# Kernel optimization log

Hardware: AMD Instinct MI355X
Metric: run time of the kernel (lower is better)

Reference implementation:

```python
import math
import jax, jax.numpy as jnp
import numpy as np

B, L, D = 1, 2048, 3072
H, KV, HD = 32, 32, 96
THETA = 10000.0
MAXP, ORIGP = 131072, 4096
ROPE_SCALE = math.sqrt(1.0 + math.log(MAXP / ORIGP) / math.log(ORIGP))
ATTN_SCALE = HD ** -0.5
OP = H * HD + 2 * KV * HD  # 9216


def setup_inputs() -> dict:
    key = jax.random.key(0)
    k1, k2, k3, k4 = jax.random.split(key, 4)
    return {
        "x": jax.random.normal(k1, (B, L, D), jnp.float32),
        "w_qkv": jax.random.normal(k2, (OP, D), jnp.float32) * (D ** -0.5),
        "w_o": jax.random.normal(k3, (D, H * HD), jnp.float32) * ((H * HD) ** -0.5),
        # Phi-3 su-scaling short factors are ~1.0; sample near 1
        "short_factor": 1.0 + 0.5 * jax.random.uniform(k4, (HD // 2,), jnp.float32),
    }


def _rotate_half(t):
    t1, t2 = jnp.split(t, 2, axis=-1)
    return jnp.concatenate([-t2, t1], axis=-1)


def reference(x, w_qkv, w_o, short_factor):
    # fused QKV projection
    qkv = x @ w_qkv.T  # [B,L,OP]
    q, k, v = jnp.split(qkv, [H * HD, H * HD + KV * HD], axis=-1)
    q = q.reshape(B, L, H, HD).transpose(0, 2, 1, 3)   # [B,H,L,HD]
    k = k.reshape(B, L, KV, HD).transpose(0, 2, 1, 3)  # [B,KV,L,HD]
    v = v.reshape(B, L, KV, HD).transpose(0, 2, 1, 3)

    # SuRoPE (always uses short_factor, matching source)
    pos = jnp.arange(L, dtype=jnp.float32)  # position_ids default arange
    inv_freq = 1.0 / (short_factor * THETA ** (jnp.arange(0, HD, 2, dtype=jnp.float32) / HD))  # [HD/2]
    freqs = pos[:, None] * inv_freq[None, :]            # [L,HD/2]
    emb = jnp.concatenate([freqs, freqs], axis=-1)      # [L,HD]
    cos = (jnp.cos(emb) * ROPE_SCALE)[None, None]       # [1,1,L,HD]
    sin = (jnp.sin(emb) * ROPE_SCALE)[None, None]
    q = q * cos + _rotate_half(q) * sin
    k = k * cos + _rotate_half(k) * sin

    # causal mask, naive attention (matches source)
    mask = jnp.triu(jnp.full((L, L), -jnp.inf, dtype=jnp.float32), 1)
    scores = jnp.einsum('bhqd,bhkd->bhqk', q * ATTN_SCALE, k) + mask
    attn = jax.nn.softmax(scores, axis=-1)
    o = jnp.einsum('bhqk,bhkd->bhqd', attn, v)
    o = o.transpose(0, 2, 1, 3).reshape(B, L, H * HD)
    return o @ w_o.T
```

## Files before the change

### kernel.cpp

```cpp
#include <hip/hip_runtime.h>
#include <math.h>

typedef __attribute__((ext_vector_type(4))) float f32x4;
typedef __attribute__((ext_vector_type(4))) float f4;
typedef __attribute__((ext_vector_type(8))) _Float16 h8;
typedef __attribute__((ext_vector_type(8))) unsigned short us8;

static __device__ __forceinline__ h8 ld8h(const _Float16* p) {
    return __builtin_bit_cast(h8, *(const us8*)p);
}
static __device__ __forceinline__ void glds16(const void* g, void* l) {
    __builtin_amdgcn_global_load_lds((const __attribute__((address_space(1))) unsigned int*)g,
                                     (__attribute__((address_space(3))) unsigned int*)l, 16, 0, 0);
}

__global__ void convert_half(const float* __restrict__ in, _Float16* __restrict__ out, int n8) {
    int i = blockIdx.x * blockDim.x + threadIdx.x;
    if (i >= n8) return;
    f4 v0 = *(const f4*)(in + (size_t)i * 8);
    f4 v1 = *(const f4*)(in + (size_t)i * 8 + 4);
    h8 o;
#pragma unroll
    for (int j = 0; j < 4; j++) {
        o[j] = (_Float16)v0[j];
        o[j + 4] = (_Float16)v1[j];
    }
    *(h8*)(out + (size_t)i * 8) = o;
}

__global__ void rope_table(const float* __restrict__ sf, float* __restrict__ cs,
                           float* __restrict__ sn, float rope_scale) {
    int i = blockIdx.x * blockDim.x + threadIdx.x;
    const int j = i % 48, l = i / 48;
    const float e = (float)(2 * j) / 96.0f;
    const float inv = 1.0f / (sf[j] * powf(10000.0f, e));
    const float ang = (float)l * inv;
    cs[i] = cosf(ang) * rope_scale;
    sn[i] = sinf(ang) * rope_scale;
}

__global__ __launch_bounds__(256, 3) void gemm_qkv(
    const _Float16* __restrict__ A, const _Float16* __restrict__ B,
    const float* __restrict__ cs, const float* __restrict__ sn,
    _Float16* __restrict__ Qh, _Float16* __restrict__ Kh, _Float16* __restrict__ Vh,
    float attn_scale) {
    const int K = 3072;
    __shared__ _Float16 As[2][128][32], Bs[2][192][32];
    const int t = threadIdx.x;
    const int lane = t & 63, w = t >> 6;
    const int bm = blockIdx.y * 128, bn = blockIdx.x * 192;
    const int wm = w >> 1, wn = w & 1;
    const int l15 = lane & 15, l4 = lane >> 4;

    int car[2], cas[2], cbr[3], cbs[3];
#pragma unroll
    for (int i = 0; i < 2; i++) {
        const int c = t + i * 256;
        car[i] = c >> 2;
        cas[i] = (((c & 3) ^ ((car[i] >> 1) & 3)) * 8);
    }
#pragma unroll
    for (int i = 0; i < 3; i++) {
        const int c = t + i * 256;
        cbr[i] = c >> 2;
        cbs[i] = (((c & 3) ^ ((cbr[i] >> 1) & 3)) * 8);
    }

    f32x4 acc[4][6] = {};

#define STG_QKV(k0_, buf)                                                              \
    {                                                                                  \
        _Float16* ab = &As[(buf)][0][0];                                               \
        _Float16* bb = &Bs[(buf)][0][0];                                               \
        _Pragma("unroll") for (int i = 0; i < 2; i++)                                  \
            glds16(A + (size_t)(bm + car[i]) * K + (k0_) + cas[i], ab + (t + i * 256) * 8); \
        _Pragma("unroll") for (int i = 0; i < 3; i++)                                  \
            glds16(B + (size_t)(bn + cbr[i]) * K + (k0_) + cbs[i], bb + (t + i * 256) * 8); \
    }

    STG_QKV(0, 0)

    int cur = 0;
    for (int k0 = 0; k0 < K; k0 += 32) {
        __syncthreads();
        if (k0 + 32 < K) STG_QKV(k0 + 32, cur ^ 1)
        h8 af[4], bf[6];
#pragma unroll
        for (int m = 0; m < 4; m++) {
            const int row = wm * 64 + m * 16 + l15;
            af[m] = ld8h(&As[cur][row][(l4 ^ ((row >> 1) & 3)) * 8]);
        }
#pragma unroll
        for (int n = 0; n < 6; n++) {
            const int row = wn * 96 + n * 16 + l15;
            bf[n] = ld8h(&Bs[cur][row][(l4 ^ ((row >> 1) & 3)) * 8]);
        }
#pragma unroll
        for (int m = 0; m < 4; m++)
#pragma unroll
            for (int n = 0; n < 6; n++)
                acc[m][n] = __builtin_amdgcn_mfma_f32_16x16x32_f16(af[m], bf[n], acc[m][n], 0, 0, 0);
        cur ^= 1;
    }
#undef STG_QKV

    const int opcol0 = bn + wn * 96;
    const int which = opcol0 / 3072;
    const int h = (opcol0 % 3072) / 96;

    if (which == 2) {
#pragma unroll
        for (int m = 0; m < 4; m++)
#pragma unroll
            for (int r = 0; r < 4; r++) {
                const int l = bm + wm * 64 + m * 16 + l4 * 4 + r;
#pragma unroll
                for (int n = 0; n < 6; n++)
                    Vh[((size_t)h * 2048 + l) * 96 + n * 16 + l15] = (_Float16)acc[m][n][r];
            }
    } else {
        _Float16* dst = (which == 0) ? Qh : Kh;
        const float qs = (which == 0) ? attn_scale : 1.0f;
#pragma unroll
        for (int m = 0; m < 4; m++)
#pragma unroll
            for (int r = 0; r < 4; r++) {
                const int l = bm + wm * 64 + m * 16 + l4 * 4 + r;
                const float* csl = cs + l * 48;
                const float* snl = sn + l * 48;
                const size_t rowb = ((size_t)h * 2048 + l) * 96;
#pragma unroll
                for (int n = 0; n < 3; n++) {
                    const int j = n * 16 + l15;
                    const float c = csl[j], s = snl[j];
                    const float lo = acc[m][n][r], hi = acc[m][n + 3][r];
                    dst[rowb + j] = (_Float16)((lo * c - hi * s) * qs);
                    dst[rowb + j + 48] = (_Float16)((hi * c + lo * s) * qs);
                }
            }
    }
}

template <typename OT>
__global__ __launch_bounds__(256, 3) void gemm_t(
    const _Float16* __restrict__ A, const _Float16* __restrict__ B,
    OT* __restrict__ C, int M, int N, int K) {
    __shared__ _Float16 As[2][128][32], Bs[2][128][32];
    const int t = threadIdx.x;
    const int lane = t & 63, w = t >> 6;
    const int bm = blockIdx.y * 128, bn = blockIdx.x * 128;
    const int wy = w >> 1, wx = w & 1;
    const int l15 = lane & 15, l4 = lane >> 4;

    const int c0 = (w * 2 + 0) * 64 + lane;
    const int c1 = (w * 2 + 1) * 64 + lane;
    const int r0s = c0 >> 2, s0 = (((c0 & 3) ^ ((r0s >> 1) & 3)) * 8);
    const int r1s = c1 >> 2, s1 = (((c1 & 3) ^ ((r1s >> 1) & 3)) * 8);

    f32x4 acc[4][4] = {};

    glds16(A + (size_t)(bm + r0s) * K + s0, &As[0][0][0] + c0 * 8);
    glds16(A + (size_t)(bm + r1s) * K + s1, &As[0][0][0] + c1 * 8);
    glds16(B + (size_t)(bn + r0s) * K + s0, &Bs[0][0][0] + c0 * 8);
    glds16(B + (size_t)(bn + r1s) * K + s1, &Bs[0][0][0] + c1 * 8);

    int cry[4], crx[4];
#pragma unroll
    for (int m = 0; m < 4; m++) {
        const int rowA = wy * 64 + m * 16 + l15;
        cry[m] = ((l4 ^ ((rowA >> 1) & 3)) * 8);
        const int rowB = wx * 64 + m * 16 + l15;
        crx[m] = ((l4 ^ ((rowB >> 1) & 3)) * 8);
    }

    int cur = 0;
    for (int k0 = 0; k0 < K; k0 += 32) {
        __syncthreads();
        const int nk = k0 + 32;
        if (nk < K) {
            _Float16* an = &As[cur ^ 1][0][0];
            _Float16* bn_ = &Bs[cur ^ 1][0][0];
            glds16(A + (size_t)(bm + r0s) * K + nk + s0, an + c0 * 8);
            glds16(A + (size_t)(bm + r1s) * K + nk + s1, an + c1 * 8);
            glds16(B + (size_t)(bn + r0s) * K + nk + s0, bn_ + c0 * 8);
            glds16(B + (size_t)(bn + r1s) * K + nk + s1, bn_ + c1 * 8);
        }
        h8 af[4], bf[4];
#pragma unroll
        for (int m = 0; m < 4; m++) af[m] = ld8h(&As[cur][wy * 64 + m * 16 + l15][cry[m]]);
#pragma unroll
        for (int n = 0; n < 4; n++) bf[n] = ld8h(&Bs[cur][wx * 64 + n * 16 + l15][crx[n]]);
#pragma unroll
        for (int m = 0; m < 4; m++)
#pragma unroll
            for (int n = 0; n < 4; n++)
                acc[m][n] = __builtin_amdgcn_mfma_f32_16x16x32_f16(af[m], bf[n], acc[m][n], 0, 0, 0);
        cur ^= 1;
    }

#pragma unroll
    for (int m = 0; m < 4; m++)
#pragma unroll
        for (int n = 0; n < 4; n++)
#pragma unroll
            for (int r = 0; r < 4; r++)
                C[(size_t)(bm + wy * 64 + m * 16 + l4 * 4 + r) * N + bn + wx * 64 + n * 16 + l15] =
                    (OT)acc[m][n][r];
}

__global__ __launch_bounds__(256) void vtrans(const _Float16* __restrict__ Vh,
                                              _Float16* __restrict__ Vt) {
    __shared__ _Float16 tile[64][105];
    const int h = blockIdx.y;
    const int l0 = blockIdx.x * 64;
    const int t = threadIdx.x;
#pragma unroll
    for (int i = 0; i < 3; i++) {
        const int v = t + i * 256;
        const int row = v / 12, seg = (v % 12) * 8;
        *(us8*)&tile[row][seg] =
            *(const us8*)(Vh + ((size_t)h * 2048 + l0 + row) * 96 + seg);
    }
    __syncthreads();
#pragma unroll
    for (int i = 0; i < 3; i++) {
        const int v = t + i * 256;
        const int d = v >> 3, lc = v & 7;
        h8 o;
#pragma unroll
        for (int j = 0; j < 8; j++) o[j] = tile[lc * 8 + j][d];
        *(h8*)(Vt + ((size_t)h * 96 + d) * 2048 + l0 + lc * 8) = o;
    }
}

__global__ __launch_bounds__(512, 2) void attn_mfma(
    const _Float16* __restrict__ Qh, const _Float16* __restrict__ Kh,
    const _Float16* __restrict__ Vt, _Float16* __restrict__ Oh) {
    __shared__ _Float16 Ks[2][64][104];
    __shared__ _Float16 Vs[2][96][72];
    __shared__ _Float16 Ps[8][16][72];

    const int h = blockIdx.y;
    const int qt = 7 - (int)blockIdx.x;
    const int q0 = qt * 256;
    const int t = threadIdx.x, lane = t & 63, w = t >> 6;
    const int l15 = lane & 15, l4 = lane >> 4;
    const int wq = q0 + w * 32;

    const _Float16* Kg = Kh + (size_t)h * 2048 * 96;
    const _Float16* Vg = Vt + (size_t)h * 96 * 2048;

    h8 qf[2][3];
#pragma unroll
    for (int g = 0; g < 2; g++) {
        const size_t qrow = ((size_t)h * 2048 + wq + g * 16 + l15) * 96;
#pragma unroll
        for (int kc = 0; kc < 3; kc++) qf[g][kc] = ld8h(Qh + qrow + kc * 32 + l4 * 8);
    }

    const int cA = t, rKA = cA / 12, sKA = (cA % 12) * 8;
    const int rVA = cA >> 3, sVA = (cA & 7) * 8;
    const int cB = 512 + t, rKB = cB / 12, sKB = (cB % 12) * 8;
    const int rVB = cB >> 3, sVB = (cB & 7) * 8;
    const bool two = (t < 256);

    us8 kregA, vregA, kregB, vregB;
    kregA = *(const us8*)(Kg + (size_t)rKA * 96 + sKA);
    vregA = *(const us8*)(Vg + (size_t)rVA * 2048 + sVA);
    if (two) {
        kregB = *(const us8*)(Kg + (size_t)rKB * 96 + sKB);
        vregB = *(const us8*)(Vg + (size_t)rVB * 2048 + sVB);
    }

    f32x4 o[2][6] = {};
    float m_i[2][4], l_i[2][4];
#pragma unroll
    for (int g = 0; g < 2; g++)
#pragma unroll
        for (int r = 0; r < 4; r++) { m_i[g][r] = -1e30f; l_i[g][r] = 0.f; }

    const int nkt = 4 * qt + 4;
    for (int kt = 0; kt < nkt; kt++) {
        const int kv0 = kt * 64;
        const int buf = kt & 1;
        *(us8*)&Ks[buf][rKA][sKA] = kregA;
        *(us8*)&Vs[buf][rVA][sVA] = vregA;
        if (two) {
            *(us8*)&Ks[buf][rKB][sKB] = kregB;
            *(us8*)&Vs[buf][rVB][sVB] = vregB;
        }
        __syncthreads();
        if (kt + 1 < nkt) {
            const int kv1 = kv0 + 64;
            kregA = *(const us8*)(Kg + (size_t)(kv1 + rKA) * 96 + sKA);
            vregA = *(const us8*)(Vg + (size_t)rVA * 2048 + kv1 + sVA);
            if (two) {
                kregB = *(const us8*)(Kg + (size_t)(kv1 + rKB) * 96 + sKB);
                vregB = *(const us8*)(Vg + (size_t)rVB * 2048 + kv1 + sVB);
            }
        }

        if (kv0 <= wq + 31) {
            f32x4 s[2][4] = {};
#pragma unroll
            for (int f = 0; f < 4; f++)
#pragma unroll
                for (int kc = 0; kc < 3; kc++) {
                    h8 kf = ld8h(&Ks[buf][f * 16 + l15][kc * 32 + l4 * 8]);
#pragma unroll
                    for (int g = 0; g < 2; g++)
                        s[g][f] = __builtin_amdgcn_mfma_f32_16x16x32_f16(qf[g][kc], kf, s[g][f], 0, 0, 0);
                }

            if (kv0 + 63 > wq) {
#pragma unroll
                for (int g = 0; g < 2; g++)
#pragma unroll
                    for (int f = 0; f < 4; f++)
#pragma unroll
                        for (int r = 0; r < 4; r++)
                            if (kv0 + f * 16 + l15 > wq + g * 16 + l4 * 4 + r) s[g][f][r] = -1e30f;
            }

            float mx[2][4];
#pragma unroll
            for (int g = 0; g < 2; g++)
#pragma unroll
                for (int r = 0; r < 4; r++) {
                    float m0 = fmaxf(fmaxf(s[g][0][r], s[g][1][r]), fmaxf(s[g][2][r], s[g][3][r]));
#pragma unroll
                    for (int msk = 1; msk < 16; msk <<= 1) m0 = fmaxf(m0, __shfl_xor(m0, msk, 64));
                    mx[g][r] = m0;
                }

            bool need = false;
#pragma unroll
            for (int g = 0; g < 2; g++)
#pragma unroll
                for (int r = 0; r < 4; r++) need = need || (mx[g][r] > m_i[g][r] + 8.0f);
            if (__any(need)) {
#pragma unroll
                for (int g = 0; g < 2; g++)
#pragma unroll
                    for (int r = 0; r < 4; r++) {
                        const float mnew = fmaxf(m_i[g][r], mx[g][r]);
                        const float sc = __expf(m_i[g][r] - mnew);
                        m_i[g][r] = mnew;
                        l_i[g][r] *= sc;
#pragma unroll
                        for (int f2 = 0; f2 < 6; f2++) o[g][f2][r] *= sc;
                    }
            }

#pragma unroll
            for (int g = 0; g < 2; g++) {
#pragma unroll
                for (int f = 0; f < 4; f++)
#pragma unroll
                    for (int r = 0; r < 4; r++) {
                        const float p = __expf(s[g][f][r] - m_i[g][r]);
                        Ps[w][l4 * 4 + r][f * 16 + l15] = (_Float16)p;
                        l_i[g][r] += p;
                    }
#pragma unroll
                for (int kc2 = 0; kc2 < 2; kc2++) {
                    h8 pa = ld8h(&Ps[w][l15][kc2 * 32 + l4 * 8]);
#pragma unroll
                    for (int f2 = 0; f2 < 6; f2++) {
                        h8 vb = ld8h(&Vs[buf][f2 * 16 + l15][kc2 * 32 + l4 * 8]);
                        o[g][f2] = __builtin_amdgcn_mfma_f32_16x16x32_f16(pa, vb, o[g][f2], 0, 0, 0);
                    }
                }
            }
        }
    }

#pragma unroll
    for (int g = 0; g < 2; g++)
#pragma unroll
        for (int r = 0; r < 4; r++) {
            float ss = l_i[g][r];
#pragma unroll
            for (int msk = 1; msk < 16; msk <<= 1) ss += __shfl_xor(ss, msk, 64);
            const float inv = 1.0f / ss;
            const size_t row = (size_t)(wq + g * 16 + l4 * 4 + r) * 3072 + h * 96;
#pragma unroll
            for (int f2 = 0; f2 < 6; f2++)
                Oh[row + f2 * 16 + l15] = (_Float16)(o[g][f2][r] * inv);
        }
}

extern "C" void kernel_launch(void* const* d_in, const int* in_sizes, int n_in,
                              void* d_out, int out_size, void* d_ws, size_t ws_size,
                              hipStream_t stream) {
    const float* x = (const float*)d_in[0];
    const float* w_qkv = (const float*)d_in[1];
    const float* w_o = (const float*)d_in[2];
    const float* sf = (const float*)d_in[3];
    float* out = (float*)d_out;
    char* ws = (char*)d_ws;

    _Float16* wqkvh = (_Float16*)(ws);
    _Float16* Qh = (_Float16*)(ws + 56623104);
    _Float16* Kh = (_Float16*)(ws + 69206016);
    _Float16* Vh = (_Float16*)(ws + 81788928);
    _Float16* Vth = (_Float16*)(ws + 94371840);
    _Float16* Oh = (_Float16*)(ws + 106954752);
    _Float16* xh = (_Float16*)(ws + 132120576);
    _Float16* woh = (_Float16*)(ws + 144703488);
    float* cs = (float*)(ws + 163577856);
    float* sn = (float*)(ws + 163971072);

    const float rope_scale = (float)sqrt(1.0 + log(131072.0 / 4096.0) / log(4096.0));
    const float attn_scale = (float)(1.0 / sqrt(96.0));

    convert_half<<<3072, 256, 0, stream>>>(x, xh, 786432);
    convert_half<<<13824, 256, 0, stream>>>(w_qkv, wqkvh, 3538944);
    rope_table<<<384, 256, 0, stream>>>(sf, cs, sn, rope_scale);
    gemm_qkv<<<dim3(48, 16), 256, 0, stream>>>(xh, wqkvh, cs, sn, Qh, Kh, Vh, attn_scale);
    vtrans<<<dim3(32, 32), 256, 0, stream>>>(Vh, Vth);
    convert_half<<<4608, 256, 0, stream>>>(w_o, woh, 1179648);
    attn_mfma<<<dim3(8, 32), 512, 0, stream>>>(Qh, Kh, Vth, Oh);
    gemm_t<float><<<dim3(24, 16), 256, 0, stream>>>(Oh, woh, out, 2048, 3072, 3072);
}
```

Baseline: 341.1 us.

## Balance causal attention with paired query tiles and retile output GEMM

The attention kernel now gives each block two 128-row query tiles, one from each end of the sequence (qt and 15-qt). This pairing evens out the causal workload across blocks. Each warp now holds 16 query rows instead of 32, which cuts register use but halves how often each K/V tile in shared memory is reused. The output projection GEMM switches from 128x128 to 128x96 tiles, giving 512 blocks instead of 384 so the device is filled more evenly.

```diff
diff --git a/kernel.cpp b/kernel.cpp
--- a/kernel.cpp
+++ b/kernel.cpp
@@ -141,71 +141,73 @@
     }
 }
 
-template <typename OT>
-__global__ __launch_bounds__(256, 3) void gemm_t(
+__global__ __launch_bounds__(256, 3) void gemm_p(
     const _Float16* __restrict__ A, const _Float16* __restrict__ B,
-    OT* __restrict__ C, int M, int N, int K) {
-    __shared__ _Float16 As[2][128][32], Bs[2][128][32];
+    float* __restrict__ C, int M, int N, int K) {
+    __shared__ _Float16 As[2][128][32], Bs[2][96][32];
     const int t = threadIdx.x;
     const int lane = t & 63, w = t >> 6;
-    const int bm = blockIdx.y * 128, bn = blockIdx.x * 128;
+    const int bm = blockIdx.y * 128, bn = blockIdx.x * 96;
     const int wy = w >> 1, wx = w & 1;
     const int l15 = lane & 15, l4 = lane >> 4;
 
-    const int c0 = (w * 2 + 0) * 64 + lane;
-    const int c1 = (w * 2 + 1) * 64 + lane;
-    const int r0s = c0 >> 2, s0 = (((c0 & 3) ^ ((r0s >> 1) & 3)) * 8);
-    const int r1s = c1 >> 2, s1 = (((c1 & 3) ^ ((r1s >> 1) & 3)) * 8);
-
-    f32x4 acc[4][4] = {};
-
-    glds16(A + (size_t)(bm + r0s) * K + s0, &As[0][0][0] + c0 * 8);
-    glds16(A + (size_t)(bm + r1s) * K + s1, &As[0][0][0] + c1 * 8);
-    glds16(B + (size_t)(bn + r0s) * K + s0, &Bs[0][0][0] + c0 * 8);
-    glds16(B + (size_t)(bn + r1s) * K + s1, &Bs[0][0][0] + c1 * 8);
-
-    int cry[4], crx[4];
-#pragma unroll
-    for (int m = 0; m < 4; m++) {
-        const int rowA = wy * 64 + m * 16 + l15;
-        cry[m] = ((l4 ^ ((rowA >> 1) & 3)) * 8);
-        const int rowB = wx * 64 + m * 16 + l15;
-        crx[m] = ((l4 ^ ((rowB >> 1) & 3)) * 8);
-    }
+    int car[2], cas[2];
+#pragma unroll
+    for (int i = 0; i < 2; i++) {
+        const int c = t + i * 256;
+        car[i] = c >> 2;
+        cas[i] = (((c & 3) ^ ((car[i] >> 1) & 3)) * 8);
+    }
+    const int cb0 = t, rb0 = cb0 >> 2, sb0 = (((cb0 & 3) ^ ((rb0 >> 1) & 3)) * 8);
+    const int cb1 = t + 256, rb1 = cb1 >> 2, sb1 = (((cb1 & 3) ^ ((rb1 >> 1) & 3)) * 8);
+    const bool bex = (t < 128);
+
+    f32x4 acc[4][3] = {};
+
+#define STG_P(k0_, buf)                                                                \
+    {                                                                                  \
+        _Float16* ab = &As[(buf)][0][0];                                               \
+        _Float16* bb = &Bs[(buf)][0][0];                                               \
+        _Pragma("unroll") for (int i = 0; i < 2; i++)                                  \
+            glds16(A + (size_t)(bm + car[i]) * K + (k0_) + cas[i], ab + (t + i * 256) * 8); \
+        glds16(B + (size_t)(bn + rb0) * K + (k0_) + sb0, bb + cb0 * 8);                \
+        if (bex) glds16(B + (size_t)(bn + rb1) * K + (k0_) + sb1, bb + cb1 * 8);       \
+    }
+
+    STG_P(0, 0)
 
     int cur = 0;
     for (int k0 = 0; k0 < K; k0 += 32) {
         __syncthreads();
-        const int nk = k0 + 32;
-        if (nk < K) {
-            _Float16* an = &As[cur ^ 1][0][0];
-            _Float16* bn_ = &Bs[cur ^ 1][0][0];
-            glds16(A + (size_t)(bm + r0s) * K + nk + s0, an + c0 * 8);
-            glds16(A + (size_t)(bm + r1s) * K + nk + s1, an + c1 * 8);
-            glds16(B + (size_t)(bn + r0s) * K + nk + s0, bn_ + c0 * 8);
-            glds16(B + (size_t)(bn + r1s) * K + nk + s1, bn_ + c1 * 8);
-        }
-        h8 af[4], bf[4];
-#pragma unroll
-        for (int m = 0; m < 4; m++) af[m] = ld8h(&As[cur][wy * 64 + m * 16 + l15][cry[m]]);
-#pragma unroll
-        for (int n = 0; n < 4; n++) bf[n] = ld8h(&Bs[cur][wx * 64 + n * 16 + l15][crx[n]]);
+        if (k0 + 32 < K) STG_P(k0 + 32, cur ^ 1)
+        h8 af[4], bf[3];
+#pragma unroll
+        for (int m = 0; m < 4; m++) {
+            const int row = wy * 64 + m * 16 + l15;
+            af[m] = ld8h(&As[cur][row][(l4 ^ ((row >> 1) & 3)) * 8]);
+        }
+#pragma unroll
+        for (int n = 0; n < 3; n++) {
+            const int row = wx * 48 + n * 16 + l15;
+            bf[n] = ld8h(&Bs[cur][row][(l4 ^ ((row >> 1) & 3)) * 8]);
+        }
 #pragma unroll
         for (int m = 0; m < 4; m++)
 #pragma unroll
-            for (int n = 0; n < 4; n++)
+            for (int n = 0; n < 3; n++)
                 acc[m][n] = __builtin_amdgcn_mfma_f32_16x16x32_f16(af[m], bf[n], acc[m][n], 0, 0, 0);
         cur ^= 1;
     }
+#undef STG_P
 
 #pragma unroll
     for (int m = 0; m < 4; m++)
 #pragma unroll
-        for (int n = 0; n < 4; n++)
+        for (int n = 0; n < 3; n++)
 #pragma unroll
             for (int r = 0; r < 4; r++)
-                C[(size_t)(bm + wy * 64 + m * 16 + l4 * 4 + r) * N + bn + wx * 64 + n * 16 + l15] =
-                    (OT)acc[m][n][r];
+                C[(size_t)(bm + wy * 64 + m * 16 + l4 * 4 + r) * N + bn + wx * 48 + n * 16 + l15] =
+                    acc[m][n][r];
 }
 
 __global__ __launch_bounds__(256) void vtrans(const _Float16* __restrict__ Vh,
@@ -241,22 +243,11 @@
     __shared__ _Float16 Ps[8][16][72];
 
     const int h = blockIdx.y;
-    const int qt = 7 - (int)blockIdx.x;
-    const int q0 = qt * 256;
     const int t = threadIdx.x, lane = t & 63, w = t >> 6;
     const int l15 = lane & 15, l4 = lane >> 4;
-    const int wq = q0 + w * 32;
 
     const _Float16* Kg = Kh + (size_t)h * 2048 * 96;
     const _Float16* Vg = Vt + (size_t)h * 96 * 2048;
-
-    h8 qf[2][3];
-#pragma unroll
-    for (int g = 0; g < 2; g++) {
-        const size_t qrow = ((size_t)h * 2048 + wq + g * 16 + l15) * 96;
-#pragma unroll
-        for (int kc = 0; kc < 3; kc++) qf[g][kc] = ld8h(Qh + qrow + kc * 32 + l4 * 8);
-    }
 
     const int cA = t, rKA = cA / 12, sKA = (cA % 12) * 8;
     const int rVA = cA >> 3, sVA = (cA & 7) * 8;
@@ -264,103 +255,98 @@
     const int rVB = cB >> 3, sVB = (cB & 7) * 8;
     const bool two = (t < 256);
 
-    us8 kregA, vregA, kregB, vregB;
-    kregA = *(const us8*)(Kg + (size_t)rKA * 96 + sKA);
-    vregA = *(const us8*)(Vg + (size_t)rVA * 2048 + sVA);
-    if (two) {
-        kregB = *(const us8*)(Kg + (size_t)rKB * 96 + sKB);
-        vregB = *(const us8*)(Vg + (size_t)rVB * 2048 + sVB);
-    }
-
-    f32x4 o[2][6] = {};
-    float m_i[2][4], l_i[2][4];
-#pragma unroll
-    for (int g = 0; g < 2; g++)
-#pragma unroll
-        for (int r = 0; r < 4; r++) { m_i[g][r] = -1e30f; l_i[g][r] = 0.f; }
-
-    const int nkt = 4 * qt + 4;
-    for (int kt = 0; kt < nkt; kt++) {
-        const int kv0 = kt * 64;
-        const int buf = kt & 1;
-        *(us8*)&Ks[buf][rKA][sKA] = kregA;
-        *(us8*)&Vs[buf][rVA][sVA] = vregA;
+    for (int ph = 0; ph < 2; ph++) {
+        const int qt = ph ? (int)blockIdx.x : 15 - (int)blockIdx.x;
+        const int q0 = qt * 128;
+        const int wq = q0 + w * 16;
+
+        h8 qf[3];
+        const size_t qrow = ((size_t)h * 2048 + wq + l15) * 96;
+#pragma unroll
+        for (int kc = 0; kc < 3; kc++) qf[kc] = ld8h(Qh + qrow + kc * 32 + l4 * 8);
+
+        us8 kregA, vregA, kregB, vregB;
+        kregA = *(const us8*)(Kg + (size_t)rKA * 96 + sKA);
+        vregA = *(const us8*)(Vg + (size_t)rVA * 2048 + sVA);
         if (two) {
-            *(us8*)&Ks[buf][rKB][sKB] = kregB;
-            *(us8*)&Vs[buf][rVB][sVB] = vregB;
-        }
-        __syncthreads();
-        if (kt + 1 < nkt) {
-            const int kv1 = kv0 + 64;
-            kregA = *(const us8*)(Kg + (size_t)(kv1 + rKA) * 96 + sKA);
-            vregA = *(const us8*)(Vg + (size_t)rVA * 2048 + kv1 + sVA);
+            kregB = *(const us8*)(Kg + (size_t)rKB * 96 + sKB);
+            vregB = *(const us8*)(Vg + (size_t)rVB * 2048 + sVB);
+        }
+
+        f32x4 o[6] = {};
+        float m_i[4] = {-1e30f, -1e30f, -1e30f, -1e30f};
+        float l_i[4] = {0.f, 0.f, 0.f, 0.f};
+
+        const int nkt = 2 * qt + 2;
+        for (int kt = 0; kt < nkt; kt++) {
+            const int kv0 = kt * 64;
+            const int buf = kt & 1;
+            *(us8*)&Ks[buf][rKA][sKA] = kregA;
+            *(us8*)&Vs[buf][rVA][sVA] = vregA;
             if (two) {
-                kregB = *(const us8*)(Kg + (size_t)(kv1 + rKB) * 96 + sKB);
-                vregB = *(const us8*)(Vg + (size_t)rVB * 2048 + kv1 + sVB);
+                *(us8*)&Ks[buf][rKB][sKB] = kregB;
+                *(us8*)&Vs[buf][rVB][sVB] = vregB;
             }
-        }
-
-        if (kv0 <= wq + 31) {
-            f32x4 s[2][4] = {};
-#pragma unroll
-            for (int f = 0; f < 4; f++)
-#pragma unroll
-                for (int kc = 0; kc < 3; kc++) {
-                    h8 kf = ld8h(&Ks[buf][f * 16 + l15][kc * 32 + l4 * 8]);
-#pragma unroll
-                    for (int g = 0; g < 2; g++)
-                        s[g][f] = __builtin_amdgcn_mfma_f32_16x16x32_f16(qf[g][kc], kf, s[g][f], 0, 0, 0);
-                }
-
-            if (kv0 + 63 > wq) {
-#pragma unroll
-                for (int g = 0; g < 2; g++)
+            __syncthreads();
+            if (kt + 1 < nkt) {
+                const int kv1 = kv0 + 64;
+                kregA = *(const us8*)(Kg + (size_t)(kv1 + rKA) * 96 + sKA);
+                vregA = *(const us8*)(Vg + (size_t)rVA * 2048 + kv1 + sVA);
+                if (two) {
+                    kregB = *(const us8*)(Kg + (size_t)(kv1 + rKB) * 96 + sKB);
+                    vregB = *(const us8*)(Vg + (size_t)rVB * 2048 + kv1 + sVB);
+                }
+            }
+
+            if (kv0 <= wq + 15) {
+                f32x4 s[4] = {};
+#pragma unroll
+                for (int f = 0; f < 4; f++)
+#pragma unroll
+                    for (int kc = 0; kc < 3; kc++) {
+                        h8 kf = ld8h(&Ks[buf][f * 16 + l15][kc * 32 + l4 * 8]);
+                        s[f] = __builtin_amdgcn_mfma_f32_16x16x32_f16(qf[kc], kf, s[f], 0, 0, 0);
+                    }
+
+                if (kv0 + 63 > wq) {
 #pragma unroll
                     for (int f = 0; f < 4; f++)
 #pragma unroll
                         for (int r = 0; r < 4; r++)
-                            if (kv0 + f * 16 + l15 > wq + g * 16 + l4 * 4 + r) s[g][f][r] = -1e30f;
-            }
-
-            float mx[2][4];
-#pragma unroll
-            for (int g = 0; g < 2; g++)
+                            if (kv0 + f * 16 + l15 > wq + l4 * 4 + r) s[f][r] = -1e30f;
+                }
+
+                float mx[4];
 #pragma unroll
                 for (int r = 0; r < 4; r++) {
-                    float m0 = fmaxf(fmaxf(s[g][0][r], s[g][1][r]), fmaxf(s[g][2][r], s[g][3][r]));
+                    float m0 = fmaxf(fmaxf(s[0][r], s[1][r]), fmaxf(s[2][r], s[3][r]));
 #pragma unroll
                     for (int msk = 1; msk < 16; msk <<= 1) m0 = fmaxf(m0, __shfl_xor(m0, msk, 64));
-                    mx[g][r] = m0;
-                }
-
-            bool need = false;
-#pragma unroll
-            for (int g = 0; g < 2; g++)
-#pragma unroll
-                for (int r = 0; r < 4; r++) need = need || (mx[g][r] > m_i[g][r] + 8.0f);
-            if (__any(need)) {
-#pragma unroll
-                for (int g = 0; g < 2; g++)
+                    mx[r] = m0;
+                }
+
+                bool need = false;
+#pragma unroll
+                for (int r = 0; r < 4; r++) need = need || (mx[r] > m_i[r] + 8.0f);
+                if (__any(need)) {
 #pragma unroll
                     for (int r = 0; r < 4; r++) {
-                        const float mnew = fmaxf(m_i[g][r], mx[g][r]);
-                        const float sc = __expf(m_i[g][r] - mnew);
-                        m_i[g][r] = mnew;
-                        l_i[g][r] *= sc;
-#pragma unroll
-                        for (int f2 = 0; f2 < 6; f2++) o[g][f2][r] *= sc;
+                        const float mnew = fmaxf(m_i[r], mx[r]);
+                        const float sc = __expf(m_i[r] - mnew);
+                        m_i[r] = mnew;
+                        l_i[r] *= sc;
+#pragma unroll
+                        for (int f2 = 0; f2 < 6; f2++) o[f2][r] *= sc;
                     }
-            }
-
-#pragma unroll
-            for (int g = 0; g < 2; g++) {
+                }
+
 #pragma unroll
                 for (int f = 0; f < 4; f++)
 #pragma unroll
                     for (int r = 0; r < 4; r++) {
-                        const float p = __expf(s[g][f][r] - m_i[g][r]);
+                        const float p = __expf(s[f][r] - m_i[r]);
                         Ps[w][l4 * 4 + r][f * 16 + l15] = (_Float16)p;
-                        l_i[g][r] += p;
+                        l_i[r] += p;
                     }
 #pragma unroll
                 for (int kc2 = 0; kc2 < 2; kc2++) {
@@ -368,26 +354,26 @@
 #pragma unroll
                     for (int f2 = 0; f2 < 6; f2++) {
                         h8 vb = ld8h(&Vs[buf][f2 * 16 + l15][kc2 * 32 + l4 * 8]);
-                        o[g][f2] = __builtin_amdgcn_mfma_f32_16x16x32_f16(pa, vb, o[g][f2], 0, 0, 0);
+                        o[f2] = __builtin_amdgcn_mfma_f32_16x16x32_f16(pa, vb, o[f2], 0, 0, 0);
                     }
                 }
             }
         }
-    }
-
-#pragma unroll
-    for (int g = 0; g < 2; g++)
+
+        __syncthreads();
+
 #pragma unroll
         for (int r = 0; r < 4; r++) {
-            float ss = l_i[g][r];
+            float ss = l_i[r];
 #pragma unroll
             for (int msk = 1; msk < 16; msk <<= 1) ss += __shfl_xor(ss, msk, 64);
             const float inv = 1.0f / ss;
-            const size_t row = (size_t)(wq + g * 16 + l4 * 4 + r) * 3072 + h * 96;
+            const size_t row = (size_t)(wq + l4 * 4 + r) * 3072 + h * 96;
 #pragma unroll
             for (int f2 = 0; f2 < 6; f2++)
-                Oh[row + f2 * 16 + l15] = (_Float16)(o[g][f2][r] * inv);
-        }
+                Oh[row + f2 * 16 + l15] = (_Float16)(o[f2][r] * inv);
+        }
+    }
 }
 
 extern "C" void kernel_launch(void* const* d_in, const int* in_sizes, int n_in,
@@ -421,5 +407,5 @@
     vtrans<<<dim3(32, 32), 256, 0, stream>>>(Vh, Vth);
     convert_half<<<4608, 256, 0, stream>>>(w_o, woh, 1179648);
     attn_mfma<<<dim3(8, 32), 512, 0, stream>>>(Qh, Kh, Vth, Oh);
-    gemm_t<float><<<dim3(24, 16), 256, 0, stream>>>(Oh, woh, out, 2048, 3072, 3072);
-}
+    gemm_p<<<dim3(32, 16), 256, 0, stream>>>(Oh, woh, out, 2048, 3072, 3072);
+}
```

New measurement: 317.6 us. 6.9% less time.
